# Performance work log

Hardware: AMD Instinct MI355X
Metric: run time of the kernel (lower is better)

Reference implementation:

```python
import jax, jax.numpy as jnp
import numpy as np
from jax import lax

GRID = 16
EPS = 1e-5


def setup_inputs() -> dict:
    key = jax.random.key(0)
    ks = jax.random.split(key, 6)
    B, Cin, H, W = 4, 3, 512, 512
    x = jax.random.normal(ks[0], (B, Cin, H, W), dtype=jnp.float32)
    w1 = jax.random.normal(ks[1], (256, Cin, 3, 3), dtype=jnp.float32) * 0.05
    b1 = jnp.zeros((256,), jnp.float32)
    bn_gamma = jnp.ones((256,), jnp.float32)
    bn_beta = jnp.zeros((256,), jnp.float32)
    bn_mean = jnp.zeros((256,), jnp.float32)
    bn_var = jnp.ones((256,), jnp.float32)
    w2 = jax.random.normal(ks[2], (128, 256), dtype=jnp.float32) * 0.05
    b2 = jnp.zeros((128,), jnp.float32)
    w3 = jax.random.normal(ks[3], (16, 128), dtype=jnp.float32) * 0.05
    b3 = jnp.zeros((16,), jnp.float32)
    return {"x": x, "w1": w1, "b1": b1, "bn_gamma": bn_gamma, "bn_beta": bn_beta,
            "bn_mean": bn_mean, "bn_var": bn_var, "w2": w2, "b2": b2, "w3": w3, "b3": b3}


def reference(x, w1, b1, bn_gamma, bn_beta, bn_mean, bn_var, w2, b2, w3, b3):
    B, _, H, W = x.shape
    # feature extractor: 3x3 conv -> BN (eval, running stats) -> ReLU
    feat = lax.conv_general_dilated(x, w1, (1, 1), 'SAME',
                                    dimension_numbers=('NCHW', 'OIHW', 'NCHW'))
    feat = feat + b1[None, :, None, None]
    inv = bn_gamma * lax.rsqrt(bn_var + EPS)
    feat = jax.nn.relu(feat * inv[None, :, None, None] + (bn_beta - bn_mean * inv)[None, :, None, None])
    # classifier: 1x1 conv -> ReLU -> 1x1 conv
    h = jax.nn.relu(jnp.einsum('bchw,oc->bohw', feat, w2) + b2[None, :, None, None])
    logits = jnp.einsum('bchw,oc->bohw', h, w3) + b3[None, :, None, None]  # [B,C,H,W]
    C = logits.shape[1]
    # grid segments: nearest upsample of grid ids == floor block assignment
    grid_h, grid_w = H // GRID, W // GRID
    S = grid_h * grid_w
    seg_row = (jnp.arange(H) * grid_h) // H
    seg_col = (jnp.arange(W) * grid_w) // W
    seg = (seg_row[:, None] * grid_w + seg_col[None, :]).reshape(-1)  # [H*W]
    # segment mean pooling (single fused scatter-add pass)
    data = logits.reshape(B, C, H * W).transpose(2, 0, 1)  # [HW,B,C]
    sums = jax.ops.segment_sum(data, seg, num_segments=S)  # [S,B,C]
    counts = jax.ops.segment_sum(jnp.ones((H * W,), logits.dtype), seg, num_segments=S)
    pooled = (sums / counts[:, None, None]).transpose(1, 2, 0)  # [B,C,S]
    # F.interpolate([B,C,S,1] -> (H,W), nearest): row h <- floor(h*S/H), col <- 0
    row_idx = (jnp.arange(H) * S) // H
    out = pooled[:, :, row_idx]  # [B,C,H]
    return jnp.broadcast_to(out[..., None], (B, C, H, W))
```

## Files before the change

### kernel.cpp

```cpp
#include <hip/hip_runtime.h>

typedef __attribute__((ext_vector_type(8))) short short8;
typedef __attribute__((ext_vector_type(4))) float f32x4;

#define MFMA(a, b, c) __builtin_amdgcn_mfma_f32_16x16x32_bf16(a, b, c, 0, 0, 0)

__device__ __forceinline__ unsigned short f2bf16(float f) {
    __bf16 h = (__bf16)f;
    return __builtin_bit_cast(unsigned short, h);
}

__device__ __forceinline__ unsigned cvtpk(float lo, float hi) {
    unsigned r;
    asm("v_cvt_pk_bf16_f32 %0, %1, %2" : "=v"(r) : "v"(lo), "v"(hi));
    return r;
}

__global__ void prep_kernel(const float* __restrict__ w1, const float* __restrict__ b1,
                            const float* __restrict__ gamma, const float* __restrict__ beta,
                            const float* __restrict__ mean, const float* __restrict__ var,
                            const float* __restrict__ w2, const float* __restrict__ w3,
                            unsigned short* __restrict__ w1a, unsigned short* __restrict__ w2a,
                            unsigned short* __restrict__ w3a) {
    int idx = blockIdx.x * 256 + threadIdx.x;
    if (idx < 8192) {
        int mt = idx >> 9, r = idx & 511, lane = r >> 3, e = r & 7;
        int o = mt * 16 + (lane & 15);
        int k = ((lane >> 4) << 3) + e;
        float inv = gamma[o] * rsqrtf(var[o] + 1e-5f);
        float v;
        if (k < 27)       v = w1[o * 27 + k] * inv;
        else if (k == 27) v = b1[o] * inv + beta[o] - mean[o] * inv;
        else              v = 0.0f;
        w1a[idx] = f2bf16(v);
    }
    if (idx < 32768) {
        int tile = idx >> 9, r = idx & 511, lane = r >> 3, e = r & 7;
        int kt = tile >> 3, mt = tile & 7;
        int g = lane >> 4;
        int o = mt * 16 + (lane & 15);
        int kphys = kt * 32 + ((e >> 2) << 4) + (g << 2) + (e & 3);
        w2a[idx] = f2bf16(w2[o * 256 + kphys]);
    }
    if (idx < 2048) {
        int kt = idx >> 9, r = idx & 511, lane = r >> 3, e = r & 7;
        int g = lane >> 4;
        int o = lane & 15;
        int kphys = kt * 32 + ((e >> 2) << 4) + (g << 2) + (e & 3);
        w3a[idx] = f2bf16(w3[o * 128 + kphys]);
    }
}

__global__ __launch_bounds__(256, 2)
void fused_block_kernel(const float* __restrict__ x,
                        const unsigned short* __restrict__ w1a,
                        const unsigned short* __restrict__ w2a,
                        const unsigned short* __restrict__ w3a,
                        const float* __restrict__ b2, const float* __restrict__ b3,
                        float* __restrict__ out) {
    __shared__ __align__(16) unsigned short w2s[32768];
    __shared__ __align__(16) unsigned short patch[3 * 18 * 18];
    __shared__ float poolW[4][16];
    __shared__ float poolF[16];

    int tid = threadIdx.x;
    int bid = blockIdx.x;
    int b  = bid >> 9;
    int br = (bid >> 4) & 31;
    int j  = bid & 15;
    int r0 = br * 16;
    int c0 = j * 32;
    int lane = tid & 63;
    int w = tid >> 6;
    int g = lane >> 4;
    int c = lane & 15;

    #pragma unroll
    for (int it = 0; it < 16; it++) {
        int off = it * 2048 + tid * 8;
        *(uint4*)&w2s[off] = *(const uint4*)&w2a[off];
    }

    for (int i = tid; i < 972; i += 256) {
        int ch = i / 324, rr = (i % 324) / 18, cc = i % 18;
        int gr = r0 + rr - 1, gc = c0 + cc - 1;
        float v = 0.0f;
        if ((unsigned)gr < 512u && (unsigned)gc < 512u)
            v = x[((b * 3 + ch) * 512 + gr) * 512 + gc];
        patch[i] = f2bf16(v);
    }
    __syncthreads();

    int offk[8];
    #pragma unroll
    for (int e = 0; e < 8; e++) {
        int k = g * 8 + e;
        int ch = (k * 7282) >> 16;
        int rem = k - ch * 9;
        int dy = (rem * 21846) >> 16;
        int dx = rem - dy * 3;
        int o = ch * 324 + dy * 18 + dx;
        offk[e] = (k < 27) ? o : 0;
    }

    short8 bfr[4];
    #pragma unroll
    for (int nj = 0; nj < 4; nj++) {
        int base = (4 * w + nj) * 18 + c;
        unsigned val[8];
        #pragma unroll
        for (int e = 0; e < 8; e++)
            val[e] = patch[base + offk[e]];
        if (g == 3) {
            val[3] = 0x3F80u;
            val[4] = val[5] = val[6] = val[7] = 0u;
        }
        union { unsigned u[4]; short8 s; } uu;
        #pragma unroll
        for (int q = 0; q < 4; q++)
            uu.u[q] = val[2 * q] | (val[2 * q + 1] << 16);
        bfr[nj] = uu.s;
    }

    const f32x4 zero = {0.f, 0.f, 0.f, 0.f};

    f32x4 acc2[8][4];
    #pragma unroll
    for (int m = 0; m < 8; m++) {
        f32x4 bb = *(const f32x4*)&b2[m * 16 + g * 4];
        #pragma unroll
        for (int nj = 0; nj < 4; nj++)
            acc2[m][nj] = bb;
    }

    #pragma unroll
    for (int hh = 0; hh < 2; hh++) {
        short8 b2fAll[4][4];
        #pragma unroll
        for (int k4 = 0; k4 < 4; k4++) {
            int kt = hh * 4 + k4;
            short8 w1f0 = *(const short8*)&w1a[(kt * 2 + 0) * 512 + lane * 8];
            short8 w1f1 = *(const short8*)&w1a[(kt * 2 + 1) * 512 + lane * 8];
            #pragma unroll
            for (int nj = 0; nj < 4; nj++) {
                f32x4 a0 = MFMA(w1f0, bfr[nj], zero);
                f32x4 a1 = MFMA(w1f1, bfr[nj], zero);
                union { unsigned u[4]; short8 s; } uu;
                uu.u[0] = cvtpk(fmaxf(a0[0], 0.f), fmaxf(a0[1], 0.f));
                uu.u[1] = cvtpk(fmaxf(a0[2], 0.f), fmaxf(a0[3], 0.f));
                uu.u[2] = cvtpk(fmaxf(a1[0], 0.f), fmaxf(a1[1], 0.f));
                uu.u[3] = cvtpk(fmaxf(a1[2], 0.f), fmaxf(a1[3], 0.f));
                b2fAll[k4][nj] = uu.s;
            }
        }
        #pragma unroll
        for (int k4 = 0; k4 < 4; k4++) {
            int kt = hh * 4 + k4;
            #pragma unroll
            for (int m = 0; m < 8; m++) {
                short8 w2f = *(const short8*)&w2s[(kt * 8 + m) * 512 + lane * 8];
                #pragma unroll
                for (int nj = 0; nj < 4; nj++)
                    acc2[m][nj] = MFMA(w2f, b2fAll[k4][nj], acc2[m][nj]);
            }
        }
    }

    f32x4 accP[4] = {zero, zero, zero, zero};
    #pragma unroll
    for (int kt = 0; kt < 4; kt++) {
        short8 w3f = *(const short8*)&w3a[kt * 512 + lane * 8];
        #pragma unroll
        for (int nj = 0; nj < 4; nj++) {
            f32x4 a0 = acc2[2 * kt + 0][nj];
            f32x4 a1 = acc2[2 * kt + 1][nj];
            union { unsigned u[4]; short8 s; } uu;
            uu.u[0] = cvtpk(fmaxf(a0[0], 0.f), fmaxf(a0[1], 0.f));
            uu.u[1] = cvtpk(fmaxf(a0[2], 0.f), fmaxf(a0[3], 0.f));
            uu.u[2] = cvtpk(fmaxf(a1[0], 0.f), fmaxf(a1[1], 0.f));
            uu.u[3] = cvtpk(fmaxf(a1[2], 0.f), fmaxf(a1[3], 0.f));
            accP[nj] = MFMA(w3f, uu.s, accP[nj]);
        }
    }

    float v0 = accP[0][0] + accP[1][0] + accP[2][0] + accP[3][0];
    float v1 = accP[0][1] + accP[1][1] + accP[2][1] + accP[3][1];
    float v2 = accP[0][2] + accP[1][2] + accP[2][2] + accP[3][2];
    float v3 = accP[0][3] + accP[1][3] + accP[2][3] + accP[3][3];
    #pragma unroll
    for (int off = 1; off < 16; off <<= 1) {
        v0 += __shfl_xor(v0, off);
        v1 += __shfl_xor(v1, off);
        v2 += __shfl_xor(v2, off);
        v3 += __shfl_xor(v3, off);
    }
    if (c == 0) {
        poolW[w][g * 4 + 0] = v0;
        poolW[w][g * 4 + 1] = v1;
        poolW[w][g * 4 + 2] = v2;
        poolW[w][g * 4 + 3] = v3;
    }
    __syncthreads();
    if (tid < 16) {
        float s = poolW[0][tid] + poolW[1][tid] + poolW[2][tid] + poolW[3][tid];
        poolF[tid] = s * (1.0f / 256.0f) + b3[tid];
    }
    __syncthreads();

    int h = r0 + j;
    int cc = tid >> 4;
    float pv = poolF[cc];
    float4 vv = {pv, pv, pv, pv};
    float4* rowp = (float4*)(out + (size_t)(((b * 16 + cc) * 512 + h)) * 512);
    int base = tid & 15;
    #pragma unroll
    for (int ii = 0; ii < 8; ii++)
        rowp[ii * 16 + base] = vv;
}

extern "C" void kernel_launch(void* const* d_in, const int* in_sizes, int n_in,
                              void* d_out, int out_size, void* d_ws, size_t ws_size,
                              hipStream_t stream) {
    const float* x     = (const float*)d_in[0];
    const float* w1    = (const float*)d_in[1];
    const float* b1    = (const float*)d_in[2];
    const float* gamma = (const float*)d_in[3];
    const float* beta  = (const float*)d_in[4];
    const float* mean  = (const float*)d_in[5];
    const float* var   = (const float*)d_in[6];
    const float* w2    = (const float*)d_in[7];
    const float* b2    = (const float*)d_in[8];
    const float* w3    = (const float*)d_in[9];
    const float* b3    = (const float*)d_in[10];
    float* out = (float*)d_out;

    unsigned short* w1a = (unsigned short*)d_ws;
    unsigned short* w2a = w1a + 8192;
    unsigned short* w3a = w2a + 32768;

    prep_kernel<<<128, 256, 0, stream>>>(w1, b1, gamma, beta, mean, var, w2, w3,
                                         w1a, w2a, w3a);
    fused_block_kernel<<<2048, 256, 0, stream>>>(x, w1a, w2a, w3a, b2, b3, out);
}
```

Baseline: 62.05 us.

## Process two tiles per 512-thread block to amortize shared w2 staging

Doubles the block size to 512 threads so each block computes two adjacent 16x32 tiles (two output rows), sharing a single LDS copy of the w2 weights. This halves the number of 64KB global-to-LDS weight loads across the grid. Launch bounds rise to 512 threads with 2 blocks per CU, which tightens the register budget for the large accumulator arrays and may cause spills or lower occupancy.

```diff
diff --git a/kernel.cpp b/kernel.cpp
--- a/kernel.cpp
+++ b/kernel.cpp
@@ -51,7 +51,7 @@
     }
 }
 
-__global__ __launch_bounds__(256, 2)
+__global__ __launch_bounds__(512, 2)
 void fused_block_kernel(const float* __restrict__ x,
                         const unsigned short* __restrict__ w1a,
                         const unsigned short* __restrict__ w2a,
@@ -59,35 +59,38 @@
                         const float* __restrict__ b2, const float* __restrict__ b3,
                         float* __restrict__ out) {
     __shared__ __align__(16) unsigned short w2s[32768];
-    __shared__ __align__(16) unsigned short patch[3 * 18 * 18];
-    __shared__ float poolW[4][16];
-    __shared__ float poolF[16];
+    __shared__ __align__(16) unsigned short patch[2][972];
+    __shared__ float poolW[8][16];
+    __shared__ float poolF[2][16];
 
     int tid = threadIdx.x;
     int bid = blockIdx.x;
-    int b  = bid >> 9;
-    int br = (bid >> 4) & 31;
-    int j  = bid & 15;
+    int b  = bid >> 8;
+    int br = (bid >> 3) & 31;
+    int jj = bid & 7;
     int r0 = br * 16;
-    int c0 = j * 32;
     int lane = tid & 63;
     int w = tid >> 6;
+    int hb = w >> 2;
+    int wl = w & 3;
     int g = lane >> 4;
     int c = lane & 15;
 
     #pragma unroll
-    for (int it = 0; it < 16; it++) {
-        int off = it * 2048 + tid * 8;
+    for (int it = 0; it < 8; it++) {
+        int off = it * 4096 + tid * 8;
         *(uint4*)&w2s[off] = *(const uint4*)&w2a[off];
     }
 
-    for (int i = tid; i < 972; i += 256) {
-        int ch = i / 324, rr = (i % 324) / 18, cc = i % 18;
-        int gr = r0 + rr - 1, gc = c0 + cc - 1;
+    for (int i = tid; i < 1944; i += 512) {
+        int t = i / 972, ii = i - t * 972;
+        int ch = ii / 324, rr = (ii % 324) / 18, cc = ii % 18;
+        int gr = r0 + rr - 1;
+        int gc = (jj * 2 + t) * 32 + cc - 1;
         float v = 0.0f;
         if ((unsigned)gr < 512u && (unsigned)gc < 512u)
             v = x[((b * 3 + ch) * 512 + gr) * 512 + gc];
-        patch[i] = f2bf16(v);
+        patch[t][ii] = f2bf16(v);
     }
     __syncthreads();
 
@@ -106,11 +109,11 @@
     short8 bfr[4];
     #pragma unroll
     for (int nj = 0; nj < 4; nj++) {
-        int base = (4 * w + nj) * 18 + c;
+        int base = (4 * wl + nj) * 18 + c;
         unsigned val[8];
         #pragma unroll
         for (int e = 0; e < 8; e++)
-            val[e] = patch[base + offk[e]];
+            val[e] = patch[hb][base + offk[e]];
         if (g == 3) {
             val[3] = 0x3F80u;
             val[4] = val[5] = val[6] = val[7] = 0u;
@@ -201,21 +204,27 @@
         poolW[w][g * 4 + 3] = v3;
     }
     __syncthreads();
-    if (tid < 16) {
-        float s = poolW[0][tid] + poolW[1][tid] + poolW[2][tid] + poolW[3][tid];
-        poolF[tid] = s * (1.0f / 256.0f) + b3[tid];
+    if (tid < 32) {
+        int t = tid >> 4, ch = tid & 15;
+        float s = poolW[4 * t + 0][ch] + poolW[4 * t + 1][ch] +
+                  poolW[4 * t + 2][ch] + poolW[4 * t + 3][ch];
+        poolF[t][ch] = s * (1.0f / 256.0f) + b3[ch];
     }
     __syncthreads();
 
-    int h = r0 + j;
-    int cc = tid >> 4;
-    float pv = poolF[cc];
-    float4 vv = {pv, pv, pv, pv};
-    float4* rowp = (float4*)(out + (size_t)(((b * 16 + cc) * 512 + h)) * 512);
-    int base = tid & 15;
-    #pragma unroll
-    for (int ii = 0; ii < 8; ii++)
-        rowp[ii * 16 + base] = vv;
+    {
+        int t = tid >> 8;
+        int r = tid & 255;
+        int cc = r >> 4;
+        int base = r & 15;
+        int h = r0 + jj * 2 + t;
+        float pv = poolF[t][cc];
+        float4 vv = {pv, pv, pv, pv};
+        float4* rowp = (float4*)(out + (size_t)(((b * 16 + cc) * 512 + h)) * 512);
+        #pragma unroll
+        for (int ii = 0; ii < 8; ii++)
+            rowp[ii * 16 + base] = vv;
+    }
 }
 
 extern "C" void kernel_launch(void* const* d_in, const int* in_sizes, int n_in,
@@ -240,5 +249,5 @@
 
     prep_kernel<<<128, 256, 0, stream>>>(w1, b1, gamma, beta, mean, var, w2, w3,
                                          w1a, w2a, w3a);
-    fused_block_kernel<<<2048, 256, 0, stream>>>(x, w1a, w2a, w3a, b2, b3, out);
-}
+    fused_block_kernel<<<1024, 512, 0, stream>>>(x, w1a, w2a, w3a, b2, b3, out);
+}
```

After: 65.55 us. 5.6% more time.
